# Optimization experiments

Hardware: AMD Instinct MI355X
Metric: run time of the kernel (lower is better)

The kernel has to match this reference:

```python
import jax, jax.numpy as jnp
import numpy as np
import math

B, HID, T, D = 4, 1024, 2048, 1024
NEG_INF = -2.0**15 + 1.0  # matches torch constant -32767.0


def setup_inputs() -> dict:
    key = jax.random.key(0)
    ks = jax.random.split(key, 9)
    s = 0.02
    return {
        "minibatch": jax.random.normal(ks[0], (B, HID, T), dtype=jnp.float32),
        "emb_w": jax.random.normal(ks[1], (D, HID), dtype=jnp.float32) * s,
        "emb_b": jax.random.normal(ks[2], (D,), dtype=jnp.float32) * s,
        "key_w": jax.random.normal(ks[3], (D, D), dtype=jnp.float32) * s,
        "key_b": jax.random.normal(ks[4], (D,), dtype=jnp.float32) * s,
        "query_w": jax.random.normal(ks[5], (D, D), dtype=jnp.float32) * s,
        "query_b": jax.random.normal(ks[6], (D,), dtype=jnp.float32) * s,
        "value_w": jax.random.normal(ks[7], (D, D), dtype=jnp.float32) * s,
        "value_b": jax.random.normal(ks[8], (D,), dtype=jnp.float32) * s,
    }


def reference(minibatch, emb_w, emb_b, key_w, key_b, query_w, query_b, value_w, value_b):
    # minibatch: [B, hidden, T] -> permute -> [B, T, hidden]
    x = jnp.transpose(minibatch, (0, 2, 1))
    m = x @ emb_w.T + emb_b                      # [B, T, D]
    keys = m @ key_w.T + key_b                   # [B, T, D]
    queries = m @ query_w.T + query_b            # [B, T, D]
    values = m @ value_w.T + value_b             # [B, T, D]
    logits = jnp.einsum('btd,bsd->bts', queries, keys)  # [B, T, T]
    mask = jnp.tril(jnp.ones((logits.shape[1], logits.shape[2]), dtype=bool))
    logits = jnp.where(mask[None], logits, jnp.float32(NEG_INF))
    # NOTE: original code applies softmax over dim=1 (query axis) and divides
    # by sqrt(d_model) AFTER the softmax — reproduced faithfully here.
    probs = jax.nn.softmax(logits, axis=1) / jnp.float32(math.sqrt(D))
    read = jnp.einsum('bts,bsd->btd', probs, values)     # [B, T, D]
    out = read + m
    return jnp.transpose(out, (0, 2, 1))                  # [B, D, T]
```

## Files before the change

### kernel.cpp

```cpp
#include <hip/hip_runtime.h>

#define T_DIM 2048
#define D_DIM 1024
#define H_DIM 1024
#define B_DIM 4

typedef __attribute__((ext_vector_type(8))) __bf16 bf16x8;
typedef __attribute__((ext_vector_type(4))) float f32x4;
typedef __attribute__((ext_vector_type(8))) unsigned short us8;

__device__ __forceinline__ unsigned short f2b(float f) {
  union { float f; unsigned int u; } x; x.f = f;
  unsigned int r = x.u + 0x7fffu + ((x.u >> 16) & 1u);
  return (unsigned short)(r >> 16);
}
__device__ __forceinline__ float b2f(unsigned short b) {
  union { unsigned int u; float f; } x; x.u = ((unsigned int)b) << 16;
  return x.f;
}

__device__ __forceinline__ void async16(unsigned short* l, const unsigned short* g) {
  __builtin_amdgcn_global_load_lds((const __attribute__((address_space(1))) void*)g,
                                   (__attribute__((address_space(3))) void*)l,
                                   16, 0, 0);
}

__global__ __launch_bounds__(256) void prep_kernel(const float* __restrict__ ew,
                                                   const float* __restrict__ kw,
                                                   const float* __restrict__ qw,
                                                   const float* __restrict__ vw,
                                                   const float* __restrict__ kb,
                                                   const float* __restrict__ qb,
                                                   const float* __restrict__ vb,
                                                   unsigned short* __restrict__ oe,
                                                   unsigned short* __restrict__ okqv,
                                                   float* __restrict__ ob) {
  int bid = blockIdx.x;
  if (bid == 4096) {
    #pragma unroll
    for (int k = 0; k < 3; k++) {
      int f4 = threadIdx.x + k * 256;
      int fi = f4 * 4;
      const float* src = fi < 1024 ? kb + fi : (fi < 2048 ? qb + (fi - 1024) : vb + (fi - 2048));
      *(float4*)(&ob[fi]) = *(const float4*)src;
    }
    return;
  }
  int i = bid * 256 + threadIdx.x;
  int seg = i >> 18;
  int off = i & 262143;
  const float* in = seg == 0 ? ew : (seg == 1 ? kw : (seg == 2 ? qw : vw));
  unsigned short* out = seg == 0 ? oe : okqv + (size_t)(seg - 1) * 1048576;
  float4 v = ((const float4*)in)[off];
  ushort4 o;
  o.x = f2b(v.x); o.y = f2b(v.y); o.z = f2b(v.z); o.w = f2b(v.w);
  ((ushort4*)out)[off] = o;
}

template <typename TIN>
__global__ __launch_bounds__(256) void transpose_kernel(const TIN* __restrict__ in,
                                                        unsigned short* __restrict__ out,
                                                        int inLD, size_t sIn, int R, size_t sOut) {
  __shared__ TIN tile[32][33];
  int c0 = blockIdx.x * 32, r0 = blockIdx.y * 32;
  int tx = threadIdx.x & 31, ty = threadIdx.x >> 5;
  const TIN* I = in + (size_t)blockIdx.z * sIn;
  #pragma unroll
  for (int i = 0; i < 32; i += 8)
    tile[ty + i][tx] = I[(size_t)(r0 + ty + i) * inLD + (c0 + tx)];
  __syncthreads();
  unsigned short* O = out + (size_t)blockIdx.z * sOut;
  #pragma unroll
  for (int i = 0; i < 32; i += 8) {
    TIN v = tile[tx][ty + i];
    unsigned short bb;
    if constexpr (sizeof(TIN) == 4) bb = f2b((float)v);
    else bb = (unsigned short)v;
    O[(size_t)(c0 + ty + i) * R + (r0 + tx)] = bb;
  }
}


#define BAR_ asm volatile("s_barrier" ::: "memory")
#define VM6_ asm volatile("s_waitcnt vmcnt(6)" ::: "memory")
#define VM4_ asm volatile("s_waitcnt vmcnt(4)" ::: "memory")
#define VM0_ asm volatile("s_waitcnt vmcnt(0)" ::: "memory")

#define STGA3(t, bb, u) async16(smem + (bb) * 24576 + (u) * 4096 + tid * 8, \
                                A + (size_t)((u) * 64 + rl0) * lda + (t) * 64 + ce)
#define STGB3(t, bb, u) async16(smem + (bb) * 24576 + 8192 + (u) * 4096 + tid * 8, \
                                Bm + (size_t)((u) * 64 + rl0) * ldb + (t) * 64 + ce)
#define STGTILE(t, bb) do { STGA3(t, bb, 0); STGA3(t, bb, 1); \
    STGB3(t, bb, 0); STGB3(t, bb, 1); STGB3(t, bb, 2); STGB3(t, bb, 3); } while (0)

#define FRG(base, row, ks) \
  (*(const bf16x8*)((base) + (row) * 64 + ((((ks) << 2) | hi) ^ (lo & 7)) * 8))

#define LOADFRAGS(bA, bB)                                            \
  _Pragma("unroll") for (int m_ = 0; m_ < 4; m_++) {                 \
    af[m_][0] = FRG(bA, wr * 64 + m_ * 16 + lo, 0);                  \
    af[m_][1] = FRG(bA, wr * 64 + m_ * 16 + lo, 1);                  \
  }                                                                  \
  _Pragma("unroll") for (int n_ = 0; n_ < 4; n_++) {                 \
    bg[n_][0] = FRG(bB, wc * 64 + n_ * 16 + lo, 0);                  \
    bg[n_][1] = FRG(bB, wc * 64 + n_ * 16 + lo, 1);                  \
  }

#define MFMA32_                                                          \
  __builtin_amdgcn_s_setprio(1);                                         \
  _Pragma("unroll") for (int ks_ = 0; ks_ < 2; ks_++)                    \
    _Pragma("unroll") for (int m_ = 0; m_ < 4; m_++)                     \
      _Pragma("unroll") for (int n_ = 0; n_ < 4; n_++)                   \
        acc[m_][n_] = __builtin_amdgcn_mfma_f32_16x16x32_bf16(           \
            af[m_][ks_], bg[n_][ks_], acc[m_][n_], 0, 0, 0);             \
  __builtin_amdgcn_s_setprio(0);

template <int OMODE, bool BIAS, int SKIP>
__global__ __launch_bounds__(512, 2)
void gemm8_kernel(const unsigned short* __restrict__ A,
                  const unsigned short* __restrict__ Bm,
                  const float* __restrict__ bias,
                  float* __restrict__ Cf, unsigned short* __restrict__ Cb,
                  int N, int K, int lda, int ldb,
                  size_t sAb, size_t sBb, size_t sCb) {
  __shared__ __align__(16) unsigned short smem[73728];

  int gx = gridDim.x;
  int nwg = gx * gridDim.y;
  int flat = blockIdx.x + gx * blockIdx.y;
  int cpx = nwg >> 3;
  int f2 = (flat & 7) * cpx + (flat >> 3);
  int bn = f2 % gx, bm = f2 / gx;
  int bz = blockIdx.z;
  if (SKIP == 1 && bn * 2 + 1 < bm) return;

  A  += (size_t)bz * sAb + (size_t)bm * 128 * lda;
  Bm += (size_t)bz * sBb + (size_t)bn * 256 * ldb;

  int tid = threadIdx.x;
  int lane = tid & 63, wid = tid >> 6;
  int wr = wid >> 2, wc = wid & 3;
  int lo = lane & 15, hi = lane >> 4;
  int rl0 = tid >> 3;
  int ce = 8 * ((tid & 7) ^ (rl0 & 7));

  int nt = K / 64;

  bf16x8 af[4][2], bg[4][2];
  f32x4 acc[4][4] = {};

  STGTILE(0, 0);
  STGTILE(1, 1);
  VM6_; BAR_;

  int cur = 0;
  for (int t = 0; t < nt - 2; t++) {
    const unsigned short* bA = smem + cur * 24576;
    const unsigned short* bB = bA + 8192;
    LOADFRAGS(bA, bB)
    int b2 = cur + 2; if (b2 >= 3) b2 -= 3;
    STGTILE(t + 2, b2);
    MFMA32_
    VM6_; BAR_;
    cur = (cur + 1 == 3) ? 0 : cur + 1;
  }
  {
    const unsigned short* bA = smem + cur * 24576;
    const unsigned short* bB = bA + 8192;
    LOADFRAGS(bA, bB)
    MFMA32_
    VM0_; BAR_;
    cur = (cur + 1 == 3) ? 0 : cur + 1;
  }
  {
    const unsigned short* bA = smem + cur * 24576;
    const unsigned short* bB = bA + 8192;
    LOADFRAGS(bA, bB)
    MFMA32_
  }

  __syncthreads();
  int row0 = bm * 128, col0 = bn * 256;
  size_t coff = (size_t)bz * sCb;

  if (OMODE == 1) {
    unsigned short* ep = smem;
    #pragma unroll
    for (int n = 0; n < 4; n++) {
      int cl = wc * 64 + n * 16 + lo;
      float bv = BIAS ? bias[col0 + cl] : 0.f;
      #pragma unroll
      for (int m = 0; m < 4; m++) {
        int rl = wr * 64 + m * 16 + hi * 4;
        #pragma unroll
        for (int j = 0; j < 4; j++)
          ep[(rl + j) * 264 + cl] = f2b(acc[m][n][j] + bv);
      }
    }
    __syncthreads();
    #pragma unroll
    for (int it = 0; it < 8; it++) {
      int idx = it * 512 + tid, r = idx >> 5, c = idx & 31;
      *(uint4*)(Cb + coff + (size_t)(row0 + r) * N + col0 + c * 8) =
          *(const uint4*)(ep + r * 264 + c * 8);
    }
  } else {
    float* ep = (float*)smem;
    #pragma unroll
    for (int half = 0; half < 2; half++) {
      __syncthreads();
      if (wr == half) {
        #pragma unroll
        for (int n = 0; n < 4; n++) {
          int cl = wc * 64 + n * 16 + lo;
          #pragma unroll
          for (int m = 0; m < 4; m++) {
            int rl = m * 16 + hi * 4;
            #pragma unroll
            for (int j = 0; j < 4; j++) ep[(rl + j) * 260 + cl] = acc[m][n][j];
          }
        }
      }
      __syncthreads();
      #pragma unroll
      for (int it = 0; it < 8; it++) {
        int idx = it * 512 + tid, r = idx >> 6, c = idx & 63;
        *(float4*)(Cf + coff + (size_t)(row0 + half * 64 + r) * N + col0 + c * 4) =
            *(const float4*)(ep + r * 260 + c * 4);
      }
    }
  }
}


#define PSTGA(t, bb, u) async16(smem + (bb) * 16384 + (u) * 4096 + tid * 8, \
                                Ap + (size_t)((u) * 64 + rl0) * T_DIM + (t) * 64 + ce)
#define PSTGB(t, bb, u) async16(smem + (bb) * 16384 + 8192 + (u) * 4096 + tid * 8, \
                                Bp + (size_t)((u) * 64 + rl0) * T_DIM + (t) * 64 + ce)
#define PSTG(t, bb) do { PSTGA(t, bb, 0); PSTGA(t, bb, 1); \
                         PSTGB(t, bb, 0); PSTGB(t, bb, 1); } while (0)

#define PVFRAGS(bA, bB)                                              \
  _Pragma("unroll") for (int m_ = 0; m_ < 4; m_++) {                 \
    af[m_][0] = FRG(bA, wr * 64 + m_ * 16 + lo, 0);                  \
    af[m_][1] = FRG(bA, wr * 64 + m_ * 16 + lo, 1);                  \
  }                                                                  \
  _Pragma("unroll") for (int n_ = 0; n_ < 2; n_++) {                 \
    bg[n_][0] = FRG(bB, wc * 32 + n_ * 16 + lo, 0);                  \
    bg[n_][1] = FRG(bB, wc * 32 + n_ * 16 + lo, 1);                  \
  }

#define PVMFMA_                                                          \
  __builtin_amdgcn_s_setprio(1);                                         \
  _Pragma("unroll") for (int ks_ = 0; ks_ < 2; ks_++)                    \
    _Pragma("unroll") for (int m_ = 0; m_ < 4; m_++)                     \
      _Pragma("unroll") for (int n_ = 0; n_ < 2; n_++)                   \
        acc[m_][n_] = __builtin_amdgcn_mfma_f32_16x16x32_bf16(           \
            af[m_][ks_], bg[n_][ks_], acc[m_][n_], 0, 0, 0);             \
  __builtin_amdgcn_s_setprio(0);

__global__ __launch_bounds__(512, 2)
void pv_kernel(const unsigned short* __restrict__ probs,
               const unsigned short* __restrict__ VT,
               const unsigned short* __restrict__ mres,
               float* __restrict__ out) {
  __shared__ __align__(16) unsigned short smem[49152];
  int bn = blockIdx.x;
  int jj = blockIdx.y;
  int bz = blockIdx.z;
  int tid = threadIdx.x;
  int lane = tid & 63, wid = tid >> 6;
  int wr = wid >> 2, wc = wid & 3;
  int lo = lane & 15, hi = lane >> 4;
  int rl0 = tid >> 3;
  int ce = 8 * ((tid & 7) ^ (rl0 & 7));

  const unsigned short* Bp = VT + (size_t)bz * D_DIM * T_DIM + (size_t)(bn * 128) * T_DIM;

  #pragma unroll 1
  for (int seg = 0; seg < 2; seg++) {
    int jt = (seg == 0) ? jj : (15 - jj);
    int nt = ((seg == 0) ? (jj + 1) : (16 - jj)) * 2;
    const unsigned short* Ap = probs + (size_t)bz * T_DIM * T_DIM + (size_t)(jt * 128) * T_DIM;

    bf16x8 af[4][2], bg[2][2];
    f32x4 acc[4][2] = {};

    PSTG(0, 0);
    PSTG(1, 1);
    VM4_; BAR_;

    int cur = 0;
    for (int t = 0; t < nt - 2; t++) {
      const unsigned short* bA = smem + cur * 16384;
      const unsigned short* bB = bA + 8192;
      PVFRAGS(bA, bB)
      int b2 = cur + 2; if (b2 >= 3) b2 -= 3;
      PSTG(t + 2, b2);
      PVMFMA_
      VM4_; BAR_;
      cur = (cur + 1 == 3) ? 0 : cur + 1;
    }
    {
      const unsigned short* bA = smem + cur * 16384;
      const unsigned short* bB = bA + 8192;
      PVFRAGS(bA, bB)
      PVMFMA_
      VM0_; BAR_;
      cur = (cur + 1 == 3) ? 0 : cur + 1;
    }
    {
      const unsigned short* bA = smem + cur * 16384;
      const unsigned short* bB = bA + 8192;
      PVFRAGS(bA, bB)
      PVMFMA_
    }

    __syncthreads();
    float* ep = (float*)smem;
    #pragma unroll
    for (int n = 0; n < 2; n++) {
      int dl = wc * 32 + n * 16 + lo;
      #pragma unroll
      for (int m = 0; m < 4; m++) {
        int tl = wr * 64 + m * 16 + hi * 4;
        #pragma unroll
        for (int j = 0; j < 4; j++) {
          float v = acc[m][n][j] +
              b2f(mres[((size_t)bz * T_DIM + jt * 128 + tl + j) * D_DIM + bn * 128 + dl]);
          ep[dl * 132 + tl + j] = v;
        }
      }
    }
    __syncthreads();
    #pragma unroll
    for (int it = 0; it < 8; it++) {
      int idx = it * 512 + tid, r = idx >> 5, c = idx & 31;
      *(float4*)(out + ((size_t)bz * D_DIM + bn * 128 + r) * T_DIM + jt * 128 + c * 4) =
          *(const float4*)(ep + r * 132 + c * 4);
    }
    __syncthreads();
  }
}

__device__ __forceinline__ float wred_max(float v) {
  #pragma unroll
  for (int o = 32; o > 0; o >>= 1) v = fmaxf(v, __shfl_down(v, o, 64));
  return v;
}
__device__ __forceinline__ float wred_sum(float v) {
  #pragma unroll
  for (int o = 32; o > 0; o >>= 1) v += __shfl_down(v, o, 64);
  return v;
}

__global__ __launch_bounds__(256) void softmax_stats_kernel(const unsigned short* __restrict__ lg,
                                                            float* __restrict__ smax,
                                                            float* __restrict__ sinv) {
  __shared__ float sb[4];
  int row = blockIdx.x;
  int s = row & (T_DIM - 1);
  us8 v = ((const us8*)(lg + (size_t)row * T_DIM))[threadIdx.x];
  int tb = threadIdx.x * 8;
  float x[8];
  float mx = -3.4e38f;
  #pragma unroll
  for (int j = 0; j < 8; j++) {
    x[j] = (tb + j >= s) ? b2f(v[j]) : -3.4e38f;
    mx = fmaxf(mx, x[j]);
  }
  mx = wred_max(mx);
  if ((threadIdx.x & 63) == 0) sb[threadIdx.x >> 6] = mx;
  __syncthreads();
  mx = fmaxf(fmaxf(sb[0], sb[1]), fmaxf(sb[2], sb[3]));
  __syncthreads();
  float sum = 0.f;
  #pragma unroll
  for (int j = 0; j < 8; j++) sum += __expf(x[j] - mx);
  sum = wred_sum(sum);
  if ((threadIdx.x & 63) == 0) sb[threadIdx.x >> 6] = sum;
  __syncthreads();
  if (threadIdx.x == 0) {
    float tot = sb[0] + sb[1] + sb[2] + sb[3];
    smax[row] = mx;
    sinv[row] = 1.0f / (tot * 32.0f);
  }
}

__global__ __launch_bounds__(256) void probs_kernel(const unsigned short* __restrict__ lg,
                                                    const float* __restrict__ smax,
                                                    const float* __restrict__ sinv,
                                                    unsigned short* __restrict__ probs) {
  int bz = blockIdx.z;
  int t0 = blockIdx.x * 32, s0 = blockIdx.y * 32;
  if (s0 >= (((t0 >> 7) + 1) << 7)) return;
  __shared__ unsigned short tile[32][33];
  int tx = threadIdx.x & 31, ty = threadIdx.x >> 5;
  const unsigned short* L = lg + (size_t)bz * T_DIM * T_DIM;
  #pragma unroll
  for (int i = 0; i < 32; i += 8)
    tile[ty + i][tx] = L[(size_t)(s0 + ty + i) * T_DIM + (t0 + tx)];
  __syncthreads();
  unsigned short* P = probs + (size_t)bz * T_DIM * T_DIM;
  #pragma unroll
  for (int i = 0; i < 32; i += 8) {
    int t = t0 + ty + i, s = s0 + tx;
    float x = b2f(tile[tx][ty + i]);
    float p = (t >= s) ? __expf(x - smax[bz * T_DIM + s]) * sinv[bz * T_DIM + s] : 0.f;
    P[(size_t)t * T_DIM + s] = f2b(p);
  }
}

extern "C" void kernel_launch(void* const* d_in, const int* in_sizes, int n_in,
                              void* d_out, int out_size, void* d_ws, size_t ws_size,
                              hipStream_t stream) {
  const float* minibatch = (const float*)d_in[0];
  const float* emb_w   = (const float*)d_in[1];
  const float* emb_b   = (const float*)d_in[2];
  const float* key_w   = (const float*)d_in[3];
  const float* key_b   = (const float*)d_in[4];
  const float* query_w = (const float*)d_in[5];
  const float* query_b = (const float*)d_in[6];
  const float* value_w = (const float*)d_in[7];
  const float* value_b = (const float*)d_in[8];
  float* out = (float*)d_out;

  char* ws = (char*)d_ws;
  const size_t MB = 1ull << 20;
  unsigned short* wbf_emb = (unsigned short*)(ws + 0 * MB);
  unsigned short* wbf_kqv = (unsigned short*)(ws + 2 * MB);
  float*          kqv_b   = (float*)(ws + 8 * MB);
  unsigned short* m_bf    = (unsigned short*)(ws + 9 * MB);
  unsigned short* KQV     = (unsigned short*)(ws + 25 * MB);
  unsigned short* VT_bf   = (unsigned short*)(ws + 73 * MB);
  unsigned short* logits_bf = (unsigned short*)(ws + 89 * MB);
  unsigned short* xT      = (unsigned short*)(ws + 153 * MB);
  unsigned short* probs   = (unsigned short*)(ws + 153 * MB);
  float*          smax    = (float*)(ws + 186 * MB);
  float*          sinv    = (float*)(ws + 186 * MB + 32768);

  const int BT = B_DIM * T_DIM;
  const size_t TT = (size_t)T_DIM * T_DIM;

  prep_kernel<<<4097, 256, 0, stream>>>(emb_w, key_w, query_w, value_w,
                                        key_b, query_b, value_b,
                                        wbf_emb, wbf_kqv, kqv_b);

  transpose_kernel<float><<<dim3(T_DIM / 32, H_DIM / 32, B_DIM), 256, 0, stream>>>(
      minibatch, xT, T_DIM, (size_t)H_DIM * T_DIM, H_DIM, (size_t)T_DIM * H_DIM);

  gemm8_kernel<1, true, 0><<<dim3(D_DIM / 256, BT / 128, 1), 512, 0, stream>>>(
      xT, wbf_emb, emb_b, nullptr, m_bf, D_DIM, H_DIM, H_DIM, H_DIM, 0, 0, 0);

  gemm8_kernel<1, true, 0><<<dim3(3072 / 256, BT / 128, 1), 512, 0, stream>>>(
      m_bf, wbf_kqv, kqv_b, nullptr, KQV, 3072, D_DIM, D_DIM, D_DIM, 0, 0, 0);

  transpose_kernel<unsigned short><<<dim3(D_DIM / 32, T_DIM / 32, B_DIM), 256, 0, stream>>>(
      KQV + 2048, VT_bf, 3072, (size_t)T_DIM * 3072, T_DIM, (size_t)D_DIM * T_DIM);

  gemm8_kernel<1, false, 1><<<dim3(T_DIM / 256, T_DIM / 128, B_DIM), 512, 0, stream>>>(
      KQV, KQV + 1024, nullptr, nullptr, logits_bf, T_DIM, D_DIM, 3072, 3072,
      (size_t)T_DIM * 3072, (size_t)T_DIM * 3072, TT);

  softmax_stats_kernel<<<BT, 256, 0, stream>>>(logits_bf, smax, sinv);

  probs_kernel<<<dim3(T_DIM / 32, T_DIM / 32, B_DIM), 256, 0, stream>>>(
      logits_bf, smax, sinv, probs);

  pv_kernel<<<dim3(8, 8, B_DIM), 512, 0, stream>>>(probs, VT_bf, m_bf, out);
}
```

Before: 210.7 us.

## Fuse input transpose into embedding GEMM and add 256x256 logits GEMM

Drops the separate fp32 transpose kernel. The embedding GEMM now reads the [B,H,T] fp32 input directly, converts it to bf16 and writes it transposed into swizzled LDS, with B staged through async copies. It also replaces the logits GEMM with a new 256x256-tile kernel that has a finer-grained interleaved pipeline and skips tiles above the diagonal. This removes a full intermediate write and read, and raises compute per loaded byte for QK^T. The cost is scalar LDS stores in the prologue and more barriers in the logits kernel.

```diff
diff --git a/kernel.cpp b/kernel.cpp
--- a/kernel.cpp
+++ b/kernel.cpp
@@ -57,34 +57,32 @@
   ((ushort4*)out)[off] = o;
 }
 
-template <typename TIN>
-__global__ __launch_bounds__(256) void transpose_kernel(const TIN* __restrict__ in,
+__global__ __launch_bounds__(256) void transpose_kernel(const unsigned short* __restrict__ in,
                                                         unsigned short* __restrict__ out,
                                                         int inLD, size_t sIn, int R, size_t sOut) {
-  __shared__ TIN tile[32][33];
+  __shared__ unsigned short tile[32][33];
   int c0 = blockIdx.x * 32, r0 = blockIdx.y * 32;
   int tx = threadIdx.x & 31, ty = threadIdx.x >> 5;
-  const TIN* I = in + (size_t)blockIdx.z * sIn;
+  const unsigned short* I = in + (size_t)blockIdx.z * sIn;
   #pragma unroll
   for (int i = 0; i < 32; i += 8)
     tile[ty + i][tx] = I[(size_t)(r0 + ty + i) * inLD + (c0 + tx)];
   __syncthreads();
   unsigned short* O = out + (size_t)blockIdx.z * sOut;
   #pragma unroll
-  for (int i = 0; i < 32; i += 8) {
-    TIN v = tile[tx][ty + i];
-    unsigned short bb;
-    if constexpr (sizeof(TIN) == 4) bb = f2b((float)v);
-    else bb = (unsigned short)v;
-    O[(size_t)(c0 + ty + i) * R + (r0 + tx)] = bb;
-  }
-}
-
+  for (int i = 0; i < 32; i += 8)
+    O[(size_t)(c0 + ty + i) * R + (r0 + tx)] = tile[tx][ty + i];
+}
 
 #define BAR_ asm volatile("s_barrier" ::: "memory")
+#define LGK0_ asm volatile("s_waitcnt lgkmcnt(0)" ::: "memory")
+#define VM8_ asm volatile("s_waitcnt vmcnt(8)" ::: "memory")
 #define VM6_ asm volatile("s_waitcnt vmcnt(6)" ::: "memory")
 #define VM4_ asm volatile("s_waitcnt vmcnt(4)" ::: "memory")
 #define VM0_ asm volatile("s_waitcnt vmcnt(0)" ::: "memory")
+
+#define FRG(base, row, ks) \
+  (*(const bf16x8*)((base) + (row) * 64 + ((((ks) << 2) | hi) ^ (lo & 7)) * 8))
 
 #define STGA3(t, bb, u) async16(smem + (bb) * 24576 + (u) * 4096 + tid * 8, \
                                 A + (size_t)((u) * 64 + rl0) * lda + (t) * 64 + ce)
@@ -92,9 +90,6 @@
                                 Bm + (size_t)((u) * 64 + rl0) * ldb + (t) * 64 + ce)
 #define STGTILE(t, bb) do { STGA3(t, bb, 0); STGA3(t, bb, 1); \
     STGB3(t, bb, 0); STGB3(t, bb, 1); STGB3(t, bb, 2); STGB3(t, bb, 3); } while (0)
-
-#define FRG(base, row, ks) \
-  (*(const bf16x8*)((base) + (row) * 64 + ((((ks) << 2) | hi) ^ (lo & 7)) * 8))
 
 #define LOADFRAGS(bA, bB)                                            \
   _Pragma("unroll") for (int m_ = 0; m_ < 4; m_++) {                 \
@@ -115,7 +110,7 @@
             af[m_][ks_], bg[n_][ks_], acc[m_][n_], 0, 0, 0);             \
   __builtin_amdgcn_s_setprio(0);
 
-template <int OMODE, bool BIAS, int SKIP>
+template <int OMODE, bool BIAS>
 __global__ __launch_bounds__(512, 2)
 void gemm8_kernel(const unsigned short* __restrict__ A,
                   const unsigned short* __restrict__ Bm,
@@ -132,7 +127,6 @@
   int f2 = (flat & 7) * cpx + (flat >> 3);
   int bn = f2 % gx, bm = f2 / gx;
   int bz = blockIdx.z;
-  if (SKIP == 1 && bn * 2 + 1 < bm) return;
 
   A  += (size_t)bz * sAb + (size_t)bm * 128 * lda;
   Bm += (size_t)bz * sBb + (size_t)bn * 256 * ldb;
@@ -232,6 +226,245 @@
   }
 }
 
+__global__ __launch_bounds__(512, 2)
+void embt_kernel(const float* __restrict__ X,
+                 const unsigned short* __restrict__ Bm,
+                 const float* __restrict__ bias,
+                 unsigned short* __restrict__ Cb) {
+  __shared__ __align__(16) unsigned short smem[73728];
+  const int ldb = 1024;
+  int gx = gridDim.x;
+  int nwg = gx * gridDim.y;
+  int flat = blockIdx.x + gx * blockIdx.y;
+  int cpx = nwg >> 3;
+  int f2x = (flat & 7) * cpx + (flat >> 3);
+  int bn = f2x % gx, bm = f2x / gx;
+  int batch = bm >> 4;
+  const float* Xb = X + (size_t)batch * H_DIM * T_DIM + (bm & 15) * 128;
+  Bm += (size_t)bn * 256 * ldb;
+
+  int tid = threadIdx.x;
+  int lane = tid & 63, wid = tid >> 6;
+  int wr = wid >> 2, wc = wid & 3;
+  int lo = lane & 15, hi = lane >> 4;
+  int rl0 = tid >> 3;
+  int ce = 8 * ((tid & 7) ^ (rl0 & 7));
+  int h_loc = tid >> 3, t_off = (tid & 7) * 16;
+
+  float fv[16];
+  #define ELOAD(t) do { \
+    const float* xs_ = Xb + (size_t)((t) * 64 + h_loc) * T_DIM + t_off;               \
+    float4 a_ = *(const float4*)xs_,      b_ = *(const float4*)(xs_ + 4);             \
+    float4 c_ = *(const float4*)(xs_ + 8), d_ = *(const float4*)(xs_ + 12);           \
+    fv[0]=a_.x; fv[1]=a_.y; fv[2]=a_.z; fv[3]=a_.w;                                   \
+    fv[4]=b_.x; fv[5]=b_.y; fv[6]=b_.z; fv[7]=b_.w;                                   \
+    fv[8]=c_.x; fv[9]=c_.y; fv[10]=c_.z; fv[11]=c_.w;                                 \
+    fv[12]=d_.x; fv[13]=d_.y; fv[14]=d_.z; fv[15]=d_.w; } while (0)
+  #define EWRITE(bb) do { \
+    unsigned short* ab_ = smem + (bb) * 24576;                                        \
+    _Pragma("unroll") for (int j_ = 0; j_ < 16; j_++) {                               \
+      int tr_ = t_off + j_;                                                           \
+      ab_[tr_ * 64 + (((h_loc >> 3) ^ (tr_ & 7)) << 3) + (h_loc & 7)] = f2b(fv[j_]);  \
+    } } while (0)
+
+  const int nt = 16;
+  bf16x8 af[4][2], bg[4][2];
+  f32x4 acc[4][4] = {};
+
+  ELOAD(0); EWRITE(0);
+  ELOAD(1); EWRITE(1);
+  ELOAD(2);
+  STGB3(0, 0, 0); STGB3(0, 0, 1); STGB3(0, 0, 2); STGB3(0, 0, 3);
+  STGB3(1, 1, 0); STGB3(1, 1, 1); STGB3(1, 1, 2); STGB3(1, 1, 3);
+  LGK0_; VM4_; BAR_;
+
+  int cur = 0;
+  for (int t = 0; t < nt - 2; t++) {
+    const unsigned short* bA = smem + cur * 24576;
+    const unsigned short* bB = bA + 8192;
+    LOADFRAGS(bA, bB)
+    int b2 = cur + 2; if (b2 >= 3) b2 -= 3;
+    EWRITE(b2);
+    if (t + 3 < nt) ELOAD(t + 3);
+    STGB3(t + 2, b2, 0); STGB3(t + 2, b2, 1); STGB3(t + 2, b2, 2); STGB3(t + 2, b2, 3);
+    MFMA32_
+    VM4_; BAR_;
+    cur = (cur + 1 == 3) ? 0 : cur + 1;
+  }
+  {
+    const unsigned short* bA = smem + cur * 24576;
+    const unsigned short* bB = bA + 8192;
+    LOADFRAGS(bA, bB)
+    MFMA32_
+    VM0_; BAR_;
+    cur = (cur + 1 == 3) ? 0 : cur + 1;
+  }
+  {
+    const unsigned short* bA = smem + cur * 24576;
+    const unsigned short* bB = bA + 8192;
+    LOADFRAGS(bA, bB)
+    MFMA32_
+  }
+
+  __syncthreads();
+  int row0 = bm * 128, col0 = bn * 256;
+  unsigned short* ep = smem;
+  #pragma unroll
+  for (int n = 0; n < 4; n++) {
+    int cl = wc * 64 + n * 16 + lo;
+    float bv = bias[col0 + cl];
+    #pragma unroll
+    for (int m = 0; m < 4; m++) {
+      int rl = wr * 64 + m * 16 + hi * 4;
+      #pragma unroll
+      for (int j = 0; j < 4; j++)
+        ep[(rl + j) * 264 + cl] = f2b(acc[m][n][j] + bv);
+    }
+  }
+  __syncthreads();
+  #pragma unroll
+  for (int it = 0; it < 8; it++) {
+    int idx = it * 512 + tid, r = idx >> 5, c = idx & 31;
+    *(uint4*)(Cb + (size_t)(row0 + r) * D_DIM + col0 + c * 8) =
+        *(const uint4*)(ep + r * 264 + c * 8);
+  }
+}
+
+#define STGAH(t, h) do { \
+    unsigned short* d_ = ldsA + ((t) & 1) * 16384 + (h) * 8192 + tid * 8;            \
+    const unsigned short* s_ = A + (size_t)((h) * 128 + rl0) * lda + (t) * 64 + ce;  \
+    async16(d_, s_); async16(d_ + 4096, s_ + (size_t)64 * lda); } while (0)
+#define STGBH(t, h) do { \
+    unsigned short* d_ = ldsB + ((t) & 1) * 16384 + (h) * 8192 + tid * 8;            \
+    const unsigned short* s_ = Bm + (size_t)((h) * 128 + rl0) * ldb + (t) * 64 + ce; \
+    async16(d_, s_); async16(d_ + 4096, s_ + (size_t)64 * ldb); } while (0)
+
+#define LDA_(bA, mb)                                                   \
+  _Pragma("unroll") for (int m_ = 0; m_ < 4; m_++) {                   \
+    int row_ = wr * 128 + ((mb) + m_) * 16 + lo;                       \
+    af[m_][0] = FRG(bA, row_, 0);                                      \
+    af[m_][1] = FRG(bA, row_, 1);                                      \
+  }
+
+#define LDB_(bB, nb, bgv)                                              \
+  _Pragma("unroll") for (int n_ = 0; n_ < 2; n_++) {                   \
+    int row_ = wc * 64 + ((nb) + n_) * 16 + lo;                        \
+    bgv[n_][0] = FRG(bB, row_, 0);                                     \
+    bgv[n_][1] = FRG(bB, row_, 1);                                     \
+  }
+
+#define MM_(mb, nb, bgv)                                                             \
+  __builtin_amdgcn_s_setprio(1);                                                     \
+  _Pragma("unroll") for (int m_ = 0; m_ < 4; m_++)                                   \
+    _Pragma("unroll") for (int n_ = 0; n_ < 2; n_++) {                               \
+      acc[(mb) + m_][(nb) + n_] = __builtin_amdgcn_mfma_f32_16x16x32_bf16(           \
+          af[m_][0], bgv[n_][0], acc[(mb) + m_][(nb) + n_], 0, 0, 0);                \
+      acc[(mb) + m_][(nb) + n_] = __builtin_amdgcn_mfma_f32_16x16x32_bf16(           \
+          af[m_][1], bgv[n_][1], acc[(mb) + m_][(nb) + n_], 0, 0, 0);                \
+    }                                                                                \
+  __builtin_amdgcn_s_setprio(0);
+
+__global__ __launch_bounds__(512, 2)
+void gemmL_kernel(const unsigned short* __restrict__ A,
+                  const unsigned short* __restrict__ Bm,
+                  unsigned short* __restrict__ Cb,
+                  int N, int K, int lda, int ldb,
+                  size_t sAb, size_t sBb, size_t sCb) {
+  __shared__ __align__(16) unsigned short smem[65536];
+  unsigned short* ldsA = smem;
+  unsigned short* ldsB = smem + 32768;
+
+  int gx = gridDim.x;
+  int nwg = gx * gridDim.y;
+  int flat = blockIdx.x + gx * blockIdx.y;
+  int cpx = nwg >> 3;
+  int f2x = (flat & 7) * cpx + (flat >> 3);
+  int bn = f2x % gx, bm = f2x / gx;
+  int bz = blockIdx.z;
+  if (bn < bm) return;
+
+  A  += (size_t)bz * sAb + (size_t)bm * 256 * lda;
+  Bm += (size_t)bz * sBb + (size_t)bn * 256 * ldb;
+
+  int tid = threadIdx.x;
+  int lane = tid & 63, wid = tid >> 6;
+  int wr = wid >> 2, wc = wid & 3;
+  int lo = lane & 15, hi = lane >> 4;
+  int rl0 = tid >> 3;
+  int ce = 8 * ((tid & 7) ^ (rl0 & 7));
+
+  int nt = K / 64;
+
+  bf16x8 af[4][2], bg0[2][2], bg1[2][2];
+  f32x4 acc[8][4] = {};
+
+  STGAH(0, 0); STGAH(0, 1); STGBH(0, 0); STGBH(0, 1);
+  STGAH(1, 0); STGAH(1, 1); STGBH(1, 0); STGBH(1, 1);
+  VM8_; BAR_;
+
+  const unsigned short* bA0 = ldsA;
+  const unsigned short* bB0 = ldsB;
+  const unsigned short* bA1 = ldsA + 16384;
+  const unsigned short* bB1 = ldsB + 16384;
+
+  int nIter = nt >> 1;
+  for (int i = 0; i < nIter; i++) {
+    bool last = (i == nIter - 1);
+    int ta = 2 * i, tb = ta + 1;
+    LDA_(bA0, 0) LDB_(bB0, 0, bg0)
+    BAR_; MM_(0, 0, bg0) BAR_;
+    LDB_(bB0, 2, bg1)
+    BAR_; MM_(0, 2, bg1) BAR_;
+    LDA_(bA0, 4)
+    if (!last) STGBH(ta + 2, 0);
+    BAR_; MM_(4, 0, bg0) BAR_;
+    if (!last) { STGAH(ta + 2, 0); STGBH(ta + 2, 1); }
+    BAR_; MM_(4, 2, bg1)
+    if (last) { VM0_; } else { VM6_; }
+    BAR_;
+    LDA_(bA1, 0) LDB_(bB1, 0, bg0)
+    if (!last) STGAH(ta + 2, 1);
+    BAR_; MM_(0, 0, bg0) BAR_;
+    LDB_(bB1, 2, bg1)
+    BAR_; MM_(0, 2, bg1) BAR_;
+    LDA_(bA1, 4)
+    if (!last) STGBH(tb + 2, 0);
+    BAR_; MM_(4, 0, bg0) BAR_;
+    if (!last) { STGAH(tb + 2, 0); STGBH(tb + 2, 1); STGAH(tb + 2, 1); }
+    BAR_; MM_(4, 2, bg1)
+    if (!last) VM8_;
+    BAR_;
+  }
+
+  __syncthreads();
+  int row0 = bm * 256, col0 = bn * 256;
+  size_t coff = (size_t)bz * sCb;
+  unsigned short* ep = smem;
+  #pragma unroll
+  for (int half = 0; half < 2; half++) {
+    __syncthreads();
+    if (wr == half) {
+      #pragma unroll
+      for (int n = 0; n < 4; n++) {
+        int cl = wc * 64 + n * 16 + lo;
+        #pragma unroll
+        for (int m = 0; m < 8; m++) {
+          int rl = m * 16 + hi * 4;
+          #pragma unroll
+          for (int j = 0; j < 4; j++)
+            ep[(rl + j) * 264 + cl] = f2b(acc[m][n][j]);
+        }
+      }
+    }
+    __syncthreads();
+    #pragma unroll
+    for (int it = 0; it < 8; it++) {
+      int idx = it * 512 + tid, r = idx >> 5, c = idx & 31;
+      *(uint4*)(Cb + coff + (size_t)(row0 + half * 128 + r) * N + col0 + c * 8) =
+          *(const uint4*)(ep + r * 264 + c * 8);
+    }
+  }
+}
 
 #define PSTGA(t, bb, u) async16(smem + (bb) * 16384 + (u) * 4096 + tid * 8, \
                                 Ap + (size_t)((u) * 64 + rl0) * T_DIM + (t) * 64 + ce)
@@ -250,6 +483,16 @@
     bg[n_][1] = FRG(bB, wc * 32 + n_ * 16 + lo, 1);                  \
   }
 
+#define PVMFMA_                                                          \
+  __builtin_amdgcn_s_setprio(1);                                         \
+  _Pragma("unroll") for (int ks_ = 0; ks_ < 2; ks_++)                    \
+    _Pragma("unroll") for (int m_ = 0; m_ < 4; m_++)                     \
+      _Pragma("unroll") for (int n_ = 0; n_ < 2; n_++)                   \
+        acc[m_][n_] = __builtin_amdgcn_mfma_f32_16x16x32_bf16(           \
+            af[m_][ks_], bg[ks_ == 0 ? 0 : 0][0], acc[m_][n_], 0, 0, 0); \
+  __builtin_amdgcn_s_setprio(0);
+
+#undef PVMFMA_
 #define PVMFMA_                                                          \
   __builtin_amdgcn_s_setprio(1);                                         \
   _Pragma("unroll") for (int ks_ = 0; ks_ < 2; ks_++)                    \
@@ -434,7 +677,6 @@
   unsigned short* KQV     = (unsigned short*)(ws + 25 * MB);
   unsigned short* VT_bf   = (unsigned short*)(ws + 73 * MB);
   unsigned short* logits_bf = (unsigned short*)(ws + 89 * MB);
-  unsigned short* xT      = (unsigned short*)(ws + 153 * MB);
   unsigned short* probs   = (unsigned short*)(ws + 153 * MB);
   float*          smax    = (float*)(ws + 186 * MB);
   float*          sinv    = (float*)(ws + 186 * MB + 32768);
@@ -446,20 +688,17 @@
                                         key_b, query_b, value_b,
                                         wbf_emb, wbf_kqv, kqv_b);
 
-  transpose_kernel<float><<<dim3(T_DIM / 32, H_DIM / 32, B_DIM), 256, 0, stream>>>(
-      minibatch, xT, T_DIM, (size_t)H_DIM * T_DIM, H_DIM, (size_t)T_DIM * H_DIM);
-
-  gemm8_kernel<1, true, 0><<<dim3(D_DIM / 256, BT / 128, 1), 512, 0, stream>>>(
-      xT, wbf_emb, emb_b, nullptr, m_bf, D_DIM, H_DIM, H_DIM, H_DIM, 0, 0, 0);
-
-  gemm8_kernel<1, true, 0><<<dim3(3072 / 256, BT / 128, 1), 512, 0, stream>>>(
+  embt_kernel<<<dim3(D_DIM / 256, BT / 128, 1), 512, 0, stream>>>(
+      minibatch, wbf_emb, emb_b, m_bf);
+
+  gemm8_kernel<1, true><<<dim3(3072 / 256, BT / 128, 1), 512, 0, stream>>>(
       m_bf, wbf_kqv, kqv_b, nullptr, KQV, 3072, D_DIM, D_DIM, D_DIM, 0, 0, 0);
 
-  transpose_kernel<unsigned short><<<dim3(D_DIM / 32, T_DIM / 32, B_DIM), 256, 0, stream>>>(
+  transpose_kernel<<<dim3(D_DIM / 32, T_DIM / 32, B_DIM), 256, 0, stream>>>(
       KQV + 2048, VT_bf, 3072, (size_t)T_DIM * 3072, T_DIM, (size_t)D_DIM * T_DIM);
 
-  gemm8_kernel<1, false, 1><<<dim3(T_DIM / 256, T_DIM / 128, B_DIM), 512, 0, stream>>>(
-      KQV, KQV + 1024, nullptr, nullptr, logits_bf, T_DIM, D_DIM, 3072, 3072,
+  gemmL_kernel<<<dim3(T_DIM / 256, T_DIM / 256, B_DIM), 512, 0, stream>>>(
+      KQV, KQV + 1024, logits_bf, T_DIM, D_DIM, 3072, 3072,
       (size_t)T_DIM * 3072, (size_t)T_DIM * 3072, TT);
 
   softmax_stats_kernel<<<BT, 256, 0, stream>>>(logits_bf, smax, sinv);
```

Result: no change. 213.1 us (+1.1%).

## Add 256x256 GEMM kernel, compute V transposed directly, drop V transpose

Applied to the files above, without the earlier changes.

Adds a new gemmL kernel that uses 256x256 tiles with double-buffered LDS and interleaves staging with the MFMA blocks. It is used for the K/Q projection and for the causal QK^T logits, with whole-tile skipping above the diagonal. V^T is now produced directly by a GEMM with swapped operands and a per-row bias, written as a D x (B*T) layout that pv_kernel reads with a new stride. This removes the separate V transpose kernel and the logits GEMM's 128-row tiles. The larger tiles raise register pressure, and coarser diagonal skipping may compute more masked work.

```diff
diff --git a/kernel.cpp b/kernel.cpp
--- a/kernel.cpp
+++ b/kernel.cpp
@@ -57,34 +57,31 @@
   ((ushort4*)out)[off] = o;
 }
 
-template <typename TIN>
-__global__ __launch_bounds__(256) void transpose_kernel(const TIN* __restrict__ in,
-                                                        unsigned short* __restrict__ out,
-                                                        int inLD, size_t sIn, int R, size_t sOut) {
-  __shared__ TIN tile[32][33];
+__global__ __launch_bounds__(256) void transpose_f32_kernel(const float* __restrict__ in,
+                                                            unsigned short* __restrict__ out,
+                                                            int inLD, size_t sIn, int R, size_t sOut) {
+  __shared__ float tile[32][33];
   int c0 = blockIdx.x * 32, r0 = blockIdx.y * 32;
   int tx = threadIdx.x & 31, ty = threadIdx.x >> 5;
-  const TIN* I = in + (size_t)blockIdx.z * sIn;
+  const float* I = in + (size_t)blockIdx.z * sIn;
   #pragma unroll
   for (int i = 0; i < 32; i += 8)
     tile[ty + i][tx] = I[(size_t)(r0 + ty + i) * inLD + (c0 + tx)];
   __syncthreads();
   unsigned short* O = out + (size_t)blockIdx.z * sOut;
   #pragma unroll
-  for (int i = 0; i < 32; i += 8) {
-    TIN v = tile[tx][ty + i];
-    unsigned short bb;
-    if constexpr (sizeof(TIN) == 4) bb = f2b((float)v);
-    else bb = (unsigned short)v;
-    O[(size_t)(c0 + ty + i) * R + (r0 + tx)] = bb;
-  }
-}
-
+  for (int i = 0; i < 32; i += 8)
+    O[(size_t)(c0 + ty + i) * R + (r0 + tx)] = f2b(tile[tx][ty + i]);
+}
 
 #define BAR_ asm volatile("s_barrier" ::: "memory")
+#define VM8_ asm volatile("s_waitcnt vmcnt(8)" ::: "memory")
 #define VM6_ asm volatile("s_waitcnt vmcnt(6)" ::: "memory")
 #define VM4_ asm volatile("s_waitcnt vmcnt(4)" ::: "memory")
 #define VM0_ asm volatile("s_waitcnt vmcnt(0)" ::: "memory")
+
+#define FRG(base, row, ks) \
+  (*(const bf16x8*)((base) + (row) * 64 + ((((ks) << 2) | hi) ^ (lo & 7)) * 8))
 
 #define STGA3(t, bb, u) async16(smem + (bb) * 24576 + (u) * 4096 + tid * 8, \
                                 A + (size_t)((u) * 64 + rl0) * lda + (t) * 64 + ce)
@@ -92,9 +89,6 @@
                                 Bm + (size_t)((u) * 64 + rl0) * ldb + (t) * 64 + ce)
 #define STGTILE(t, bb) do { STGA3(t, bb, 0); STGA3(t, bb, 1); \
     STGB3(t, bb, 0); STGB3(t, bb, 1); STGB3(t, bb, 2); STGB3(t, bb, 3); } while (0)
-
-#define FRG(base, row, ks) \
-  (*(const bf16x8*)((base) + (row) * 64 + ((((ks) << 2) | hi) ^ (lo & 7)) * 8))
 
 #define LOADFRAGS(bA, bB)                                            \
   _Pragma("unroll") for (int m_ = 0; m_ < 4; m_++) {                 \
@@ -115,14 +109,13 @@
             af[m_][ks_], bg[n_][ks_], acc[m_][n_], 0, 0, 0);             \
   __builtin_amdgcn_s_setprio(0);
 
-template <int OMODE, bool BIAS, int SKIP>
+template <int OMODE>
 __global__ __launch_bounds__(512, 2)
 void gemm8_kernel(const unsigned short* __restrict__ A,
                   const unsigned short* __restrict__ Bm,
                   const float* __restrict__ bias,
-                  float* __restrict__ Cf, unsigned short* __restrict__ Cb,
-                  int N, int K, int lda, int ldb,
-                  size_t sAb, size_t sBb, size_t sCb) {
+                  unsigned short* __restrict__ Cb,
+                  int N, int K, int lda, int ldb) {
   __shared__ __align__(16) unsigned short smem[73728];
 
   int gx = gridDim.x;
@@ -131,11 +124,9 @@
   int cpx = nwg >> 3;
   int f2 = (flat & 7) * cpx + (flat >> 3);
   int bn = f2 % gx, bm = f2 / gx;
-  int bz = blockIdx.z;
-  if (SKIP == 1 && bn * 2 + 1 < bm) return;
-
-  A  += (size_t)bz * sAb + (size_t)bm * 128 * lda;
-  Bm += (size_t)bz * sBb + (size_t)bn * 256 * ldb;
+
+  A  += (size_t)bm * 128 * lda;
+  Bm += (size_t)bn * 256 * ldb;
 
   int tid = threadIdx.x;
   int lane = tid & 63, wid = tid >> 6;
@@ -181,62 +172,173 @@
 
   __syncthreads();
   int row0 = bm * 128, col0 = bn * 256;
+  unsigned short* ep = smem;
+  #pragma unroll
+  for (int n = 0; n < 4; n++) {
+    int cl = wc * 64 + n * 16 + lo;
+    float bvc = (OMODE == 1) ? bias[col0 + cl] : 0.f;
+    #pragma unroll
+    for (int m = 0; m < 4; m++) {
+      int rl = wr * 64 + m * 16 + hi * 4;
+      #pragma unroll
+      for (int j = 0; j < 4; j++) {
+        float bv = (OMODE == 3) ? bias[row0 + rl + j] : bvc;
+        ep[(rl + j) * 264 + cl] = f2b(acc[m][n][j] + bv);
+      }
+    }
+  }
+  __syncthreads();
+  #pragma unroll
+  for (int it = 0; it < 8; it++) {
+    int idx = it * 512 + tid, r = idx >> 5, c = idx & 31;
+    *(uint4*)(Cb + (size_t)(row0 + r) * N + col0 + c * 8) =
+        *(const uint4*)(ep + r * 264 + c * 8);
+  }
+}
+
+#define STGAH(t, h) do { \
+    unsigned short* d_ = ldsA + ((t) & 1) * 16384 + (h) * 8192 + tid * 8;            \
+    const unsigned short* s_ = A + (size_t)((h) * 128 + rl0) * lda + (t) * 64 + ce;  \
+    async16(d_, s_); async16(d_ + 4096, s_ + (size_t)64 * lda); } while (0)
+#define STGBH(t, h) do { \
+    unsigned short* d_ = ldsB + ((t) & 1) * 16384 + (h) * 8192 + tid * 8;            \
+    const unsigned short* s_ = Bm + (size_t)((h) * 128 + rl0) * ldb + (t) * 64 + ce; \
+    async16(d_, s_); async16(d_ + 4096, s_ + (size_t)64 * ldb); } while (0)
+
+#define LDA_(bA, mb)                                                   \
+  _Pragma("unroll") for (int m_ = 0; m_ < 4; m_++) {                   \
+    int row_ = wr * 128 + ((mb) + m_) * 16 + lo;                       \
+    af[m_][0] = FRG(bA, row_, 0);                                      \
+    af[m_][1] = FRG(bA, row_, 1);                                      \
+  }
+
+#define LDB_(bB, nb, bgv)                                              \
+  _Pragma("unroll") for (int n_ = 0; n_ < 2; n_++) {                   \
+    int row_ = wc * 64 + ((nb) + n_) * 16 + lo;                        \
+    bgv[n_][0] = FRG(bB, row_, 0);                                     \
+    bgv[n_][1] = FRG(bB, row_, 1);                                     \
+  }
+
+#define MM_(mb, nb, bgv)                                                             \
+  __builtin_amdgcn_s_setprio(1);                                                     \
+  _Pragma("unroll") for (int m_ = 0; m_ < 4; m_++)                                   \
+    _Pragma("unroll") for (int n_ = 0; n_ < 2; n_++) {                               \
+      acc[(mb) + m_][(nb) + n_] = __builtin_amdgcn_mfma_f32_16x16x32_bf16(           \
+          af[m_][0], bgv[n_][0], acc[(mb) + m_][(nb) + n_], 0, 0, 0);                \
+      acc[(mb) + m_][(nb) + n_] = __builtin_amdgcn_mfma_f32_16x16x32_bf16(           \
+          af[m_][1], bgv[n_][1], acc[(mb) + m_][(nb) + n_], 0, 0, 0);                \
+    }                                                                                \
+  __builtin_amdgcn_s_setprio(0);
+
+template <bool BIAS, bool SKIP>
+__global__ __launch_bounds__(512, 2)
+void gemmL_kernel(const unsigned short* __restrict__ A,
+                  const unsigned short* __restrict__ Bm,
+                  const float* __restrict__ bias,
+                  unsigned short* __restrict__ Cb,
+                  int N, int K, int lda, int ldb,
+                  size_t sAb, size_t sBb, size_t sCb) {
+  __shared__ __align__(16) unsigned short smem[65536];
+  unsigned short* ldsA = smem;
+  unsigned short* ldsB = smem + 32768;
+
+  int gx = gridDim.x;
+  int nwg = gx * gridDim.y;
+  int flat = blockIdx.x + gx * blockIdx.y;
+  int cpx = nwg >> 3;
+  int f2x = (flat & 7) * cpx + (flat >> 3);
+  int bn = f2x % gx, bm = f2x / gx;
+  int bz = blockIdx.z;
+  if (SKIP && bn < bm) return;
+
+  A  += (size_t)bz * sAb + (size_t)bm * 256 * lda;
+  Bm += (size_t)bz * sBb + (size_t)bn * 256 * ldb;
+
+  int tid = threadIdx.x;
+  int lane = tid & 63, wid = tid >> 6;
+  int wr = wid >> 2, wc = wid & 3;
+  int lo = lane & 15, hi = lane >> 4;
+  int rl0 = tid >> 3;
+  int ce = 8 * ((tid & 7) ^ (rl0 & 7));
+
+  int nt = K / 64;
+
+  bf16x8 af[4][2], bg0[2][2], bg1[2][2];
+  f32x4 acc[8][4] = {};
+
+  STGAH(0, 0); STGAH(0, 1); STGBH(0, 0); STGBH(0, 1);
+  STGAH(1, 0); STGAH(1, 1); STGBH(1, 0); STGBH(1, 1);
+  VM8_; BAR_;
+
+  const unsigned short* bA0 = ldsA;
+  const unsigned short* bB0 = ldsB;
+  const unsigned short* bA1 = ldsA + 16384;
+  const unsigned short* bB1 = ldsB + 16384;
+
+  int nIter = nt >> 1;
+  for (int i = 0; i < nIter; i++) {
+    bool last = (i == nIter - 1);
+    int ta = 2 * i, tb = ta + 1;
+    LDA_(bA0, 0) LDB_(bB0, 0, bg0)
+    BAR_; MM_(0, 0, bg0) BAR_;
+    LDB_(bB0, 2, bg1)
+    BAR_; MM_(0, 2, bg1) BAR_;
+    LDA_(bA0, 4)
+    if (!last) STGBH(ta + 2, 0);
+    BAR_; MM_(4, 0, bg0) BAR_;
+    if (!last) { STGAH(ta + 2, 0); STGBH(ta + 2, 1); }
+    BAR_; MM_(4, 2, bg1)
+    if (last) { VM0_; } else { VM6_; }
+    BAR_;
+    LDA_(bA1, 0) LDB_(bB1, 0, bg0)
+    if (!last) STGAH(ta + 2, 1);
+    BAR_; MM_(0, 0, bg0) BAR_;
+    LDB_(bB1, 2, bg1)
+    BAR_; MM_(0, 2, bg1) BAR_;
+    LDA_(bA1, 4)
+    if (!last) STGBH(tb + 2, 0);
+    BAR_; MM_(4, 0, bg0) BAR_;
+    if (!last) { STGAH(tb + 2, 0); STGBH(tb + 2, 1); STGAH(tb + 2, 1); }
+    BAR_; MM_(4, 2, bg1)
+    if (!last) VM8_;
+    BAR_;
+  }
+
+  __syncthreads();
+  int row0 = bm * 256, col0 = bn * 256;
   size_t coff = (size_t)bz * sCb;
-
-  if (OMODE == 1) {
-    unsigned short* ep = smem;
-    #pragma unroll
-    for (int n = 0; n < 4; n++) {
-      int cl = wc * 64 + n * 16 + lo;
-      float bv = BIAS ? bias[col0 + cl] : 0.f;
+  unsigned short* ep = smem;
+  #pragma unroll
+  for (int half = 0; half < 2; half++) {
+    __syncthreads();
+    if (wr == half) {
       #pragma unroll
-      for (int m = 0; m < 4; m++) {
-        int rl = wr * 64 + m * 16 + hi * 4;
+      for (int n = 0; n < 4; n++) {
+        int cl = wc * 64 + n * 16 + lo;
+        float bv = BIAS ? bias[col0 + cl] : 0.f;
         #pragma unroll
-        for (int j = 0; j < 4; j++)
-          ep[(rl + j) * 264 + cl] = f2b(acc[m][n][j] + bv);
+        for (int m = 0; m < 8; m++) {
+          int rl = m * 16 + hi * 4;
+          #pragma unroll
+          for (int j = 0; j < 4; j++)
+            ep[(rl + j) * 264 + cl] = f2b(acc[m][n][j] + bv);
+        }
       }
     }
     __syncthreads();
     #pragma unroll
     for (int it = 0; it < 8; it++) {
       int idx = it * 512 + tid, r = idx >> 5, c = idx & 31;
-      *(uint4*)(Cb + coff + (size_t)(row0 + r) * N + col0 + c * 8) =
+      *(uint4*)(Cb + coff + (size_t)(row0 + half * 128 + r) * N + col0 + c * 8) =
           *(const uint4*)(ep + r * 264 + c * 8);
     }
-  } else {
-    float* ep = (float*)smem;
-    #pragma unroll
-    for (int half = 0; half < 2; half++) {
-      __syncthreads();
-      if (wr == half) {
-        #pragma unroll
-        for (int n = 0; n < 4; n++) {
-          int cl = wc * 64 + n * 16 + lo;
-          #pragma unroll
-          for (int m = 0; m < 4; m++) {
-            int rl = m * 16 + hi * 4;
-            #pragma unroll
-            for (int j = 0; j < 4; j++) ep[(rl + j) * 260 + cl] = acc[m][n][j];
-          }
-        }
-      }
-      __syncthreads();
-      #pragma unroll
-      for (int it = 0; it < 8; it++) {
-        int idx = it * 512 + tid, r = idx >> 6, c = idx & 63;
-        *(float4*)(Cf + coff + (size_t)(row0 + half * 64 + r) * N + col0 + c * 4) =
-            *(const float4*)(ep + r * 260 + c * 4);
-      }
-    }
-  }
-}
-
+  }
+}
 
 #define PSTGA(t, bb, u) async16(smem + (bb) * 16384 + (u) * 4096 + tid * 8, \
                                 Ap + (size_t)((u) * 64 + rl0) * T_DIM + (t) * 64 + ce)
 #define PSTGB(t, bb, u) async16(smem + (bb) * 16384 + 8192 + (u) * 4096 + tid * 8, \
-                                Bp + (size_t)((u) * 64 + rl0) * T_DIM + (t) * 64 + ce)
+                                Bp + (size_t)((u) * 64 + rl0) * 8192 + (t) * 64 + ce)
 #define PSTG(t, bb) do { PSTGA(t, bb, 0); PSTGA(t, bb, 1); \
                          PSTGB(t, bb, 0); PSTGB(t, bb, 1); } while (0)
 
@@ -261,7 +363,7 @@
 
 __global__ __launch_bounds__(512, 2)
 void pv_kernel(const unsigned short* __restrict__ probs,
-               const unsigned short* __restrict__ VT,
+               const unsigned short* __restrict__ VTd,
                const unsigned short* __restrict__ mres,
                float* __restrict__ out) {
   __shared__ __align__(16) unsigned short smem[49152];
@@ -275,7 +377,7 @@
   int rl0 = tid >> 3;
   int ce = 8 * ((tid & 7) ^ (rl0 & 7));
 
-  const unsigned short* Bp = VT + (size_t)bz * D_DIM * T_DIM + (size_t)(bn * 128) * T_DIM;
+  const unsigned short* Bp = VTd + (size_t)(bn * 128) * 8192 + bz * T_DIM;
 
   #pragma unroll 1
   for (int seg = 0; seg < 2; seg++) {
@@ -431,8 +533,8 @@
   unsigned short* wbf_kqv = (unsigned short*)(ws + 2 * MB);
   float*          kqv_b   = (float*)(ws + 8 * MB);
   unsigned short* m_bf    = (unsigned short*)(ws + 9 * MB);
-  unsigned short* KQV     = (unsigned short*)(ws + 25 * MB);
-  unsigned short* VT_bf   = (unsigned short*)(ws + 73 * MB);
+  unsigned short* KQ      = (unsigned short*)(ws + 25 * MB);
+  unsigned short* VTd     = (unsigned short*)(ws + 57 * MB);
   unsigned short* logits_bf = (unsigned short*)(ws + 89 * MB);
   unsigned short* xT      = (unsigned short*)(ws + 153 * MB);
   unsigned short* probs   = (unsigned short*)(ws + 153 * MB);
@@ -446,26 +548,26 @@
                                         key_b, query_b, value_b,
                                         wbf_emb, wbf_kqv, kqv_b);
 
-  transpose_kernel<float><<<dim3(T_DIM / 32, H_DIM / 32, B_DIM), 256, 0, stream>>>(
+  transpose_f32_kernel<<<dim3(T_DIM / 32, H_DIM / 32, B_DIM), 256, 0, stream>>>(
       minibatch, xT, T_DIM, (size_t)H_DIM * T_DIM, H_DIM, (size_t)T_DIM * H_DIM);
 
-  gemm8_kernel<1, true, 0><<<dim3(D_DIM / 256, BT / 128, 1), 512, 0, stream>>>(
-      xT, wbf_emb, emb_b, nullptr, m_bf, D_DIM, H_DIM, H_DIM, H_DIM, 0, 0, 0);
-
-  gemm8_kernel<1, true, 0><<<dim3(3072 / 256, BT / 128, 1), 512, 0, stream>>>(
-      m_bf, wbf_kqv, kqv_b, nullptr, KQV, 3072, D_DIM, D_DIM, D_DIM, 0, 0, 0);
-
-  transpose_kernel<unsigned short><<<dim3(D_DIM / 32, T_DIM / 32, B_DIM), 256, 0, stream>>>(
-      KQV + 2048, VT_bf, 3072, (size_t)T_DIM * 3072, T_DIM, (size_t)D_DIM * T_DIM);
-
-  gemm8_kernel<1, false, 1><<<dim3(T_DIM / 256, T_DIM / 128, B_DIM), 512, 0, stream>>>(
-      KQV, KQV + 1024, nullptr, nullptr, logits_bf, T_DIM, D_DIM, 3072, 3072,
-      (size_t)T_DIM * 3072, (size_t)T_DIM * 3072, TT);
+  gemm8_kernel<1><<<dim3(D_DIM / 256, BT / 128, 1), 512, 0, stream>>>(
+      xT, wbf_emb, emb_b, m_bf, D_DIM, H_DIM, H_DIM, H_DIM);
+
+  gemmL_kernel<true, false><<<dim3(2048 / 256, BT / 256, 1), 512, 0, stream>>>(
+      m_bf, wbf_kqv, kqv_b, KQ, 2048, D_DIM, D_DIM, D_DIM, 0, 0, 0);
+
+  gemm8_kernel<3><<<dim3(BT / 256, D_DIM / 128, 1), 512, 0, stream>>>(
+      wbf_kqv + 2 * 1024 * 1024, m_bf, value_b, VTd, BT, D_DIM, D_DIM, D_DIM);
+
+  gemmL_kernel<false, true><<<dim3(T_DIM / 256, T_DIM / 256, B_DIM), 512, 0, stream>>>(
+      KQ, KQ + 1024, nullptr, logits_bf, T_DIM, D_DIM, 2048, 2048,
+      (size_t)T_DIM * 2048, (size_t)T_DIM * 2048, TT);
 
   softmax_stats_kernel<<<BT, 256, 0, stream>>>(logits_bf, smax, sinv);
 
   probs_kernel<<<dim3(T_DIM / 32, T_DIM / 32, B_DIM), 256, 0, stream>>>(
       logits_bf, smax, sinv, probs);
 
-  pv_kernel<<<dim3(8, 8, B_DIM), 512, 0, stream>>>(probs, VT_bf, m_bf, out);
-}
+  pv_kernel<<<dim3(8, 8, B_DIM), 512, 0, stream>>>(probs, VTd, m_bf, out);
+}
```

Result: faster. 194.8 us (-7.5%).
